# Performance work log

Hardware: AMD Instinct MI355X
Metric: run time of the kernel (lower is better)

The kernel has to match this reference:

```python
import jax, jax.numpy as jnp
import numpy as np

N, E = 50000, 400000
IC, OC, WIDTH, DEPTH = 128, 128, 2, 3


def setup_inputs() -> dict:
    key = jax.random.key(0)
    ks = jax.random.split(key, 9)
    s = 0.02
    return {
        "node_tensor": jax.random.normal(ks[0], (N, 1, IC), jnp.float32),
        "edge_index": jax.random.randint(ks[1], (2, E), 0, N, dtype=jnp.int32),
        "W_pre": jax.random.normal(ks[2], (IC, OC * WIDTH), jnp.float32) * s,
        "b_pre": jax.random.normal(ks[3], (OC * WIDTH,), jnp.float32) * s,
        "W_merge": jax.random.normal(ks[4], (IC, OC * WIDTH), jnp.float32) * s,
        "b_merge": jax.random.normal(ks[5], (OC * WIDTH,), jnp.float32) * s,
        "W_conv": jax.random.normal(ks[6], (WIDTH, OC, OC), jnp.float32) * s,
        "b_conv": jax.random.normal(ks[7], (OC * WIDTH,), jnp.float32) * s,
    }


def reference(node_tensor, edge_index, W_pre, b_pre, W_merge, b_merge, W_conv, b_conv):
    n = node_tensor.shape[0]
    nodes = node_tensor[:, 0, :]                       # (N, IC)

    src, dst = edge_index[0], edge_index[1]
    deg = jax.ops.segment_sum(jnp.ones((E,), node_tensor.dtype), dst, num_segments=n)
    norm = jnp.where(deg > 0, jax.lax.rsqrt(jnp.maximum(deg, 1.0)), 0.0)  # D^{-1/2}

    def laplacian_action(x):                           # x: (N, C); L_sym x
        agg = jax.ops.segment_sum(norm[src, None] * x[src], dst, num_segments=n)
        return x - norm[:, None] * agg

    merge = nodes @ W_merge + b_merge                  # (N, OC*W)
    out = jax.nn.relu(nodes @ W_pre + b_pre + merge)   # (N, OC*W)

    for _ in range(DEPTH - 1):
        out = out - laplacian_action(out)
        # grouped 1x1 conv: width contiguous groups of OC channels
        h = out.reshape(n, WIDTH, OC)
        h = jnp.einsum("nwi,woi->nwo", h, W_conv).reshape(n, WIDTH * OC) + b_conv
        out = jax.nn.relu(h + merge)

    # final (N, OC, W) reshape + adaptive_avg_pool1d(1) == mean over width
    out = out.reshape(n, OC, WIDTH).mean(axis=-1)
    return out[:, :, None]                             # (N, OC, 1)
```

## Files before the change

kernel.cpp:

```cpp
#include <hip/hip_runtime.h>

typedef unsigned short u16;
typedef unsigned char u8;
typedef __attribute__((ext_vector_type(8))) short bf16x8;
typedef __attribute__((ext_vector_type(4))) float f32x4;
typedef __attribute__((ext_vector_type(2))) float f32x2;

#define ICNST 128
#define C2 256

__device__ __forceinline__ float bf2f(u16 u){
  return __uint_as_float(((unsigned int)u) << 16);
}
__device__ __forceinline__ u16 f2bf(float f){
  unsigned int u = __float_as_uint(f);
  unsigned int r = (u + 0x7fffu + ((u >> 16) & 1u)) >> 16;
  return (u16)r;
}
__device__ __forceinline__ unsigned int pk2(float a, float b){
  return (unsigned int)f2bf(a) | ((unsigned int)f2bf(b) << 16);
}

#if defined(__has_builtin)
#if __has_builtin(__builtin_amdgcn_cvt_pk_f32_fp8) && __has_builtin(__builtin_amdgcn_cvt_pk_fp8_f32)
#define HAVE_FP8_BUILTINS 1
#endif
#endif

#ifndef HAVE_FP8_BUILTINS
__device__ __forceinline__ float fp8tof(unsigned int b){
  unsigned int sgn = (b & 0x80u) << 24;
  unsigned int em = b & 0x7fu;
  float mag;
  if (em >= 8u){
    unsigned int e = em >> 3, m = em & 7u;
    mag = __uint_as_float(((e + 120u) << 23) | (m << 20));
  } else {
    mag = (float)em * 0.001953125f;
  }
  return __uint_as_float(__float_as_uint(mag) | sgn);
}
__device__ __forceinline__ unsigned int ftofp8(float f){
  unsigned int u = __float_as_uint(f);
  unsigned int s = (u >> 24) & 0x80u;
  float a = __uint_as_float(u & 0x7fffffffu);
  if (a > 448.f) a = 448.f;
  if (a < 0.015625f){
    int q = (int)(a * 512.f + 0.5f);
    return s | (unsigned int)q;
  }
  int e; float m = frexpf(a, &e);
  int q = (int)(m * 16.f + 0.5f);
  if (q == 16){ q = 8; e += 1; }
  int E = e - 1 + 7;
  if (E > 15){ E = 15; q = 14; }
  return s | (unsigned int)((E << 3) | (q & 7));
}
#endif

template<bool HI>
__device__ __forceinline__ f32x2 up2(unsigned int v){
#ifdef HAVE_FP8_BUILTINS
  return __builtin_amdgcn_cvt_pk_f32_fp8(v, HI);
#else
  f32x2 r;
  constexpr unsigned int sh = HI ? 16u : 0u;
  r.x = fp8tof((v >> sh) & 0xffu);
  r.y = fp8tof((v >> (sh + 8u)) & 0xffu);
  return r;
#endif
}
__device__ __forceinline__ unsigned int pk4fp8(float a, float b, float c, float d){
#ifdef HAVE_FP8_BUILTINS
  unsigned int o = (unsigned int)__builtin_amdgcn_cvt_pk_fp8_f32(a, b, 0, false);
  o = (unsigned int)__builtin_amdgcn_cvt_pk_fp8_f32(c, d, (int)o, true);
  return o;
#else
  return ftofp8(a) | (ftofp8(b) << 8) | (ftofp8(c) << 16) | (ftofp8(d) << 24);
#endif
}

__global__ __launch_bounds__(512) void k_zero(int* __restrict__ deg, int n){
  int i = blockIdx.x * 512 + threadIdx.x;
  if (i < n) deg[i] = 0;
}

__global__ __launch_bounds__(256) void k_pre(const int* __restrict__ dst,
    int* __restrict__ deg, const float* __restrict__ Wpre,
    const float* __restrict__ Wmrg, const float* __restrict__ Wcv,
    u16* __restrict__ WT, u16* __restrict__ Wc, int E){
  int bid = blockIdx.x;
  if (bid < 384){
    int idx = bid * 256 + threadIdx.x;
    if (idx < 65536){
      int j = idx & 511, k = idx >> 9;
      float v = (j < 256) ? Wpre[k * 256 + j] : Wmrg[k * 256 + (j - 256)];
      WT[j * 128 + k] = f2bf(v);
    } else if (idx < 65536 + 32768){
      int x = idx - 65536;
      Wc[x] = f2bf(Wcv[x]);
    }
  } else {
    int e = (bid - 384) * 256 + threadIdx.x;
    if (e < E) atomicAdd(&deg[dst[e]], 1);
  }
}

__global__ __launch_bounds__(256) void k_scan1(const int* __restrict__ deg,
    int* __restrict__ bsum, int n){
  __shared__ int red[256];
  int t = threadIdx.x;
  int i = blockIdx.x * 256 + t;
  red[t] = (i < n) ? deg[i] : 0;
  __syncthreads();
  for (int off = 128; off > 0; off >>= 1){
    if (t < off) red[t] += red[t + off];
    __syncthreads();
  }
  if (t == 0) bsum[blockIdx.x] = red[0];
}

__global__ __launch_bounds__(256) void k_scan2(int* __restrict__ bsum, int nb){
  __shared__ int s[256];
  int t = threadIdx.x;
  int v = (t < nb) ? bsum[t] : 0;
  s[t] = v;
  __syncthreads();
  for (int off = 1; off < 256; off <<= 1){
    int u = (t >= off) ? s[t - off] : 0;
    __syncthreads();
    s[t] += u;
    __syncthreads();
  }
  if (t < nb) bsum[t] = s[t] - v;
}

__global__ __launch_bounds__(256) void k_scan3(const int* __restrict__ deg,
    const int* __restrict__ bsum, int* __restrict__ row_start,
    int* __restrict__ cursor, float* __restrict__ norm, int n){
  __shared__ int s[256];
  int t = threadIdx.x;
  int i = blockIdx.x * 256 + t;
  int v = (i < n) ? deg[i] : 0;
  s[t] = v;
  __syncthreads();
  for (int off = 1; off < 256; off <<= 1){
    int u = (t >= off) ? s[t - off] : 0;
    __syncthreads();
    s[t] += u;
    __syncthreads();
  }
  int ex = s[t] - v + bsum[blockIdx.x];
  if (i < n){
    row_start[i] = ex;
    cursor[i] = ex;
    norm[i] = (v > 0) ? rsqrtf((float)v) : 0.f;
    if (i == n - 1) row_start[n] = ex + v;
  }
}

__global__ void k_scatter(const int* __restrict__ src, const int* __restrict__ dstA,
    int* __restrict__ cursor, int* __restrict__ csr_src, int E){
  int e = blockIdx.x * blockDim.x + threadIdx.x;
  if (e < E){
    int d = dstA[e];
    int pos = atomicAdd(&cursor[d], 1);
    csr_src[pos] = src[e];
  }
}

__global__ __launch_bounds__(512) void k_initM(const float* __restrict__ node,
    const u16* __restrict__ WT, const float* __restrict__ bpre,
    const float* __restrict__ bmrg, const float* __restrict__ norm,
    u16* __restrict__ merge, u8* __restrict__ outA, int n){
  __shared__ u16 Al[64 * 128];
  int t = threadIdx.x;
  int w = t >> 6, l = t & 63;
  int n0 = blockIdx.x * 64;
  int cb = w * 32;
  int lk = (l >> 4) * 8;

  float nr4[4];
  #pragma unroll
  for (int fr = 0; fr < 4; ++fr){
    int row = n0 + fr * 16 + (l & 15);
    nr4[fr] = (row < n) ? norm[row] : 0.f;
  }
  float4 bPr[2], bMr[2];
  #pragma unroll
  for (int fcp = 0; fcp < 2; ++fcp){
    int j0 = cb + fcp * 16 + (l >> 4) * 4;
    bPr[fcp] = *(const float4*)(bpre + j0);
    bMr[fcp] = *(const float4*)(bmrg + j0);
  }

  {
    int row = t >> 3, c0 = (t & 7) * 16;
    const float* src = node + (size_t)(n0 + row) * ICNST + c0;
    bool ok = (n0 + row) < n;
    #pragma unroll
    for (int q = 0; q < 4; ++q){
      float4 v = ok ? *(const float4*)(src + q * 4) : float4{0.f, 0.f, 0.f, 0.f};
      int byte = (row * 256 + c0 * 2 + q * 8) ^ ((row & 7) << 4);
      uint2 pp; pp.x = pk2(v.x, v.y); pp.y = pk2(v.z, v.w);
      *(uint2*)((char*)Al + byte) = pp;
    }
  }
  __syncthreads();

  f32x4 acc[4][4] = {};
  #pragma unroll
  for (int ks = 0; ks < 4; ++ks){
    bf16x8 bf[4];
    #pragma unroll
    for (int fc = 0; fc < 4; ++fc){
      int j = (fc < 2) ? (cb + fc * 16 + (l & 15))
                       : (256 + cb + (fc - 2) * 16 + (l & 15));
      bf[fc] = *(const bf16x8*)(WT + (size_t)j * 128 + ks * 32 + lk);
    }
    bf16x8 af[4];
    #pragma unroll
    for (int fr = 0; fr < 4; ++fr){
      int row = fr * 16 + (l & 15);
      int byte = (row * 256 + ks * 64 + (l >> 4) * 16) ^ ((l & 7) << 4);
      af[fr] = *(const bf16x8*)((const char*)Al + byte);
    }
    #pragma unroll
    for (int fr = 0; fr < 4; ++fr)
      #pragma unroll
      for (int fc = 0; fc < 4; ++fc)
        acc[fr][fc] = __builtin_amdgcn_mfma_f32_16x16x32_bf16(bf[fc], af[fr], acc[fr][fc], 0, 0, 0);
  }

  #pragma unroll
  for (int fr = 0; fr < 4; ++fr){
    int row = n0 + fr * 16 + (l & 15);
    bool ok = row < n;
    float nr = nr4[fr];
    #pragma unroll
    for (int fcp = 0; fcp < 2; ++fcp){
      int j0 = cb + fcp * 16 + (l >> 4) * 4;
      f32x4 aP = acc[fr][fcp], aM = acc[fr][fcp + 2];
      float bPe[4] = {bPr[fcp].x, bPr[fcp].y, bPr[fcp].z, bPr[fcp].w};
      float bMe[4] = {bMr[fcp].x, bMr[fcp].y, bMr[fcp].z, bMr[fcp].w};
      ushort4 mgv;
      u16* mgp = (u16*)&mgv;
      float o4[4];
      #pragma unroll
      for (int r = 0; r < 4; ++r){
        float mg = aM[r] + bMe[r];
        float o  = aP[r] + bPe[r] + mg;
        o = (o > 0.f) ? o : 0.f;
        mgp[r] = f2bf(mg);
        o4[r] = nr * o;
      }
      if (ok){
        *(ushort4*)(merge + (size_t)row * C2 + j0) = mgv;
        *(unsigned int*)(outA + (size_t)row * C2 + j0) = pk4fp8(o4[0], o4[1], o4[2], o4[3]);
      }
    }
  }
}

template<int FINAL>
__global__ __launch_bounds__(512) void k_pconv(const u8* __restrict__ src,
    const int* __restrict__ row_start, const int* __restrict__ csr,
    const float* __restrict__ norm,
    const u16* __restrict__ Wc, const float* __restrict__ bc,
    const u16* __restrict__ merge,
    u8* __restrict__ dstB, float* __restrict__ out, int n, int Etot){
  __shared__ u16 Al[64 * 256];
  int t = threadIdx.x;
  int w = t >> 6, l = t & 63;
  int n0 = blockIdx.x * 64;
  int wh = w >> 2;
  int lk = (l >> 4) * 8;
  int q = l >> 4;
  int c16 = l & 15;

  float nr4[4];
  #pragma unroll
  for (int fr = 0; fr < 4; ++fr){
    int row = n0 + fr * 16 + (l & 15);
    nr4[fr] = (row < n) ? norm[row] : 0.f;
  }
  float4 bCr[2];
  #pragma unroll
  for (int fc = 0; fc < 2; ++fc)
    bCr[fc] = *(const float4*)(bc + w * 32 + fc * 16 + (l >> 4) * 4);

  const u8* Ac = src + (size_t)c16 * 16;
  int rbase = w * 8 + q * 2;
  float acc16[2][16];
  int bb[2], ee[2];
  float ndk[2];
  #pragma unroll
  for (int k = 0; k < 2; ++k){
    int gw = n0 + rbase + k;
    bool ok = gw < n;
    bb[k] = ok ? row_start[gw] : 0;
    ee[k] = ok ? row_start[gw + 1] : 0;
    ndk[k] = ok ? norm[gw] : 0.f;
    #pragma unroll
    for (int m = 0; m < 16; ++m) acc16[k][m] = 0.f;
  }
  int Em1 = Etot - 1;
  bool more = (bb[0] < ee[0]) | (bb[1] < ee[1]);
  while (__any(more)){
    uint4 rr[2];
    float wk[2];
    #pragma unroll
    for (int k = 0; k < 2; ++k){
      bool v = bb[k] < ee[k];
      wk[k] = v ? 1.f : 0.f;
      int idx = (bb[k] < Em1) ? bb[k] : Em1;
      int s0 = csr[idx];
      rr[k] = *(const uint4*)(Ac + (size_t)s0 * C2);
      bb[k] += v ? 1 : 0;
    }
    #pragma unroll
    for (int k = 0; k < 2; ++k){
      f32x2 p;
      p = up2<false>(rr[k].x); acc16[k][ 0] = fmaf(wk[k], p.x, acc16[k][ 0]); acc16[k][ 1] = fmaf(wk[k], p.y, acc16[k][ 1]);
      p = up2<true >(rr[k].x); acc16[k][ 2] = fmaf(wk[k], p.x, acc16[k][ 2]); acc16[k][ 3] = fmaf(wk[k], p.y, acc16[k][ 3]);
      p = up2<false>(rr[k].y); acc16[k][ 4] = fmaf(wk[k], p.x, acc16[k][ 4]); acc16[k][ 5] = fmaf(wk[k], p.y, acc16[k][ 5]);
      p = up2<true >(rr[k].y); acc16[k][ 6] = fmaf(wk[k], p.x, acc16[k][ 6]); acc16[k][ 7] = fmaf(wk[k], p.y, acc16[k][ 7]);
      p = up2<false>(rr[k].z); acc16[k][ 8] = fmaf(wk[k], p.x, acc16[k][ 8]); acc16[k][ 9] = fmaf(wk[k], p.y, acc16[k][ 9]);
      p = up2<true >(rr[k].z); acc16[k][10] = fmaf(wk[k], p.x, acc16[k][10]); acc16[k][11] = fmaf(wk[k], p.y, acc16[k][11]);
      p = up2<false>(rr[k].w); acc16[k][12] = fmaf(wk[k], p.x, acc16[k][12]); acc16[k][13] = fmaf(wk[k], p.y, acc16[k][13]);
      p = up2<true >(rr[k].w); acc16[k][14] = fmaf(wk[k], p.x, acc16[k][14]); acc16[k][15] = fmaf(wk[k], p.y, acc16[k][15]);
    }
    more = (bb[0] < ee[0]) | (bb[1] < ee[1]);
  }
  #pragma unroll
  for (int k = 0; k < 2; ++k){
    int rl = rbase + k;
    float nd = ndk[k];
    uint4 v0, v1;
    v0.x = pk2(nd * acc16[k][ 0], nd * acc16[k][ 1]);
    v0.y = pk2(nd * acc16[k][ 2], nd * acc16[k][ 3]);
    v0.z = pk2(nd * acc16[k][ 4], nd * acc16[k][ 5]);
    v0.w = pk2(nd * acc16[k][ 6], nd * acc16[k][ 7]);
    v1.x = pk2(nd * acc16[k][ 8], nd * acc16[k][ 9]);
    v1.y = pk2(nd * acc16[k][10], nd * acc16[k][11]);
    v1.z = pk2(nd * acc16[k][12], nd * acc16[k][13]);
    v1.w = pk2(nd * acc16[k][14], nd * acc16[k][15]);
    int base2 = rl * 512 + c16 * 32;
    int sw = (rl & 7) << 4;
    *(uint4*)((char*)Al + (base2 ^ sw)) = v0;
    *(uint4*)((char*)Al + ((base2 + 16) ^ sw)) = v1;
  }
  __syncthreads();

  f32x4 acc[4][2] = {};
  #pragma unroll
  for (int ks = 0; ks < 4; ++ks){
    bf16x8 bf[2];
    #pragma unroll
    for (int fc = 0; fc < 2; ++fc){
      int rw = w * 32 + fc * 16 + (l & 15);
      bf[fc] = *(const bf16x8*)(Wc + (size_t)rw * 128 + ks * 32 + lk);
    }
    bf16x8 af[4];
    #pragma unroll
    for (int fr = 0; fr < 4; ++fr){
      int row = fr * 16 + (l & 15);
      int byte = (row * 512 + wh * 256 + ks * 64 + (l >> 4) * 16) ^ ((l & 7) << 4);
      af[fr] = *(const bf16x8*)((const char*)Al + byte);
    }
    #pragma unroll
    for (int fr = 0; fr < 4; ++fr)
      #pragma unroll
      for (int fc = 0; fc < 2; ++fc)
        acc[fr][fc] = __builtin_amdgcn_mfma_f32_16x16x32_bf16(bf[fc], af[fr], acc[fr][fc], 0, 0, 0);
  }

  #pragma unroll
  for (int fr = 0; fr < 4; ++fr){
    int row = n0 + fr * 16 + (l & 15);
    bool ok = row < n;
    float nr = nr4[fr];
    #pragma unroll
    for (int fc = 0; fc < 2; ++fc){
      int j0 = w * 32 + fc * 16 + (l >> 4) * 4;
      ushort4 mg4 = ok ? *(const ushort4*)(merge + (size_t)row * C2 + j0)
                       : ushort4{0, 0, 0, 0};
      const u16* mge = (const u16*)&mg4;
      float bCe[4] = {bCr[fc].x, bCr[fc].y, bCr[fc].z, bCr[fc].w};
      float v[4];
      #pragma unroll
      for (int r = 0; r < 4; ++r){
        float o = acc[fr][fc][r] + bCe[r] + bf2f(mge[r]);
        v[r] = (o > 0.f) ? o : 0.f;
      }
      if (ok){
        if (!FINAL){
          *(unsigned int*)(dstB + (size_t)row * C2 + j0) =
              pk4fp8(nr * v[0], nr * v[1], nr * v[2], nr * v[3]);
        } else {
          float2 om;
          om.x = 0.5f * (v[0] + v[1]);
          om.y = 0.5f * (v[2] + v[3]);
          *(float2*)(out + (size_t)row * 128 + (j0 >> 1)) = om;
        }
      }
    }
  }
}

extern "C" void kernel_launch(void* const* d_in, const int* in_sizes, int n_in,
                              void* d_out, int out_size, void* d_ws, size_t ws_size,
                              hipStream_t stream){
  const float* node = (const float*)d_in[0];
  const int*   eidx = (const int*)d_in[1];
  const float* Wpre = (const float*)d_in[2];
  const float* bpre = (const float*)d_in[3];
  const float* Wmrg = (const float*)d_in[4];
  const float* bmrg = (const float*)d_in[5];
  const float* Wcv  = (const float*)d_in[6];
  const float* bcv  = (const float*)d_in[7];
  float* out = (float*)d_out;

  const int n = in_sizes[0] / ICNST;
  const int E = in_sizes[1] / 2;
  const int* srcp = eidx;
  const int* dstp = eidx + E;

  char* ws = (char*)d_ws;
  size_t off = 0;
  auto alloc = [&](size_t bytes) -> char* {
    char* p = ws + off;
    off += bytes;
    off = (off + 255) & ~(size_t)255;
    return p;
  };
  int*   deg       = (int*)  alloc((size_t)n * 4);
  float* norm      = (float*)alloc((size_t)n * 4);
  int*   row_start = (int*)  alloc((size_t)(n + 1) * 4);
  int*   cursor    = (int*)  alloc((size_t)n * 4);
  int*   csr       = (int*)  alloc((size_t)E * 4);
  u16*   merge     = (u16*)  alloc((size_t)n * C2 * 2);
  u8*    bufA      = (u8*)   alloc((size_t)n * C2);
  u8*    bufB      = (u8*)   alloc((size_t)n * C2);
  u16*   WT        = (u16*)  alloc((size_t)512 * 128 * 2);
  u16*   Wcbf      = (u16*)  alloc((size_t)2 * 128 * 128 * 2);
  int*   bsum      = (int*)  alloc((size_t)256 * 4);
  (void)ws_size; (void)n_in; (void)out_size;

  const int nb = (n + 255) / 256;

  k_zero<<<(n + 511) / 512, 512, 0, stream>>>(deg, n);
  k_pre<<<384 + (E + 255) / 256, 256, 0, stream>>>(dstp, deg, Wpre, Wmrg, Wcv, WT, Wcbf, E);
  k_scan1<<<nb, 256, 0, stream>>>(deg, bsum, n);
  k_scan2<<<1, 256, 0, stream>>>(bsum, nb);
  k_scan3<<<nb, 256, 0, stream>>>(deg, bsum, row_start, cursor, norm, n);
  k_scatter<<<(E + 255) / 256, 256, 0, stream>>>(srcp, dstp, cursor, csr, E);

  int gb64 = (n + 63) / 64;
  k_initM<<<gb64, 512, 0, stream>>>(node, WT, bpre, bmrg, norm, merge, bufA, n);

  k_pconv<0><<<gb64, 512, 0, stream>>>(bufA, row_start, csr, norm, Wcbf, bcv, merge, bufB, nullptr, n, E);
  k_pconv<1><<<gb64, 512, 0, stream>>>(bufB, row_start, csr, norm, Wcbf, bcv, merge, nullptr, out, n, E);
}
```

Baseline: 192.3 us.

## Fuse graph preprocessing kernels into one cooperative kernel with grid syncs

Replaces the zero, weight-conversion/degree, three scan and scatter kernels with a single cooperative kernel on a fixed 256x256 grid. Phases are separated by grid-wide barriers. The aim is to remove several kernel launches and their inter-kernel gaps. In exchange it adds five grid syncs and relies on cooperative launch, with a fixed grid that limits parallelism for the edge passes.

```diff
diff --git a/kernel.cpp b/kernel.cpp
--- a/kernel.cpp
+++ b/kernel.cpp
@@ -1,4 +1,7 @@
 #include <hip/hip_runtime.h>
+#include <hip/hip_cooperative_groups.h>
+
+namespace cg = cooperative_groups;
 
 typedef unsigned short u16;
 typedef unsigned char u8;
@@ -80,50 +83,37 @@
 #endif
 }
 
-__global__ __launch_bounds__(512) void k_zero(int* __restrict__ deg, int n){
-  int i = blockIdx.x * 512 + threadIdx.x;
-  if (i < n) deg[i] = 0;
-}
-
-__global__ __launch_bounds__(256) void k_pre(const int* __restrict__ dst,
+__global__ void k_prep(const int* __restrict__ srcp, const int* __restrict__ dstp,
     int* __restrict__ deg, const float* __restrict__ Wpre,
     const float* __restrict__ Wmrg, const float* __restrict__ Wcv,
-    u16* __restrict__ WT, u16* __restrict__ Wc, int E){
-  int bid = blockIdx.x;
-  if (bid < 384){
-    int idx = bid * 256 + threadIdx.x;
-    if (idx < 65536){
-      int j = idx & 511, k = idx >> 9;
-      float v = (j < 256) ? Wpre[k * 256 + j] : Wmrg[k * 256 + (j - 256)];
-      WT[j * 128 + k] = f2bf(v);
-    } else if (idx < 65536 + 32768){
-      int x = idx - 65536;
-      Wc[x] = f2bf(Wcv[x]);
-    }
-  } else {
-    int e = (bid - 384) * 256 + threadIdx.x;
-    if (e < E) atomicAdd(&deg[dst[e]], 1);
-  }
-}
-
-__global__ __launch_bounds__(256) void k_scan1(const int* __restrict__ deg,
-    int* __restrict__ bsum, int n){
-  __shared__ int red[256];
-  int t = threadIdx.x;
-  int i = blockIdx.x * 256 + t;
-  red[t] = (i < n) ? deg[i] : 0;
-  __syncthreads();
-  for (int off = 128; off > 0; off >>= 1){
-    if (t < off) red[t] += red[t + off];
-    __syncthreads();
-  }
-  if (t == 0) bsum[blockIdx.x] = red[0];
-}
-
-__global__ __launch_bounds__(256) void k_scan2(int* __restrict__ bsum, int nb){
+    u16* __restrict__ WT, u16* __restrict__ Wc,
+    int* __restrict__ row_start, int* __restrict__ cursor,
+    float* __restrict__ norm, int* __restrict__ bsum,
+    int* __restrict__ csr, int n, int E){
+  cg::grid_group grid = cg::this_grid();
   __shared__ int s[256];
-  int t = threadIdx.x;
-  int v = (t < nb) ? bsum[t] : 0;
+  __shared__ int s2[256];
+  int t = threadIdx.x, b = blockIdx.x;
+  int gid = b * 256 + t;
+  const int gsz = 256 * 256;
+
+  for (int i = gid; i < n; i += gsz) deg[i] = 0;
+  grid.sync();
+
+  {
+    int i = gid;
+    int j = i & 511, k = i >> 9;
+    float v = (j < 256) ? Wpre[k * 256 + j] : Wmrg[k * 256 + (j - 256)];
+    WT[j * 128 + k] = f2bf(v);
+  }
+  if (gid < 32768) Wc[gid] = f2bf(Wcv[gid]);
+  for (int e = gid; e < E; e += gsz) atomicAdd(&deg[dstp[e]], 1);
+  grid.sync();
+
+  int C = (n + 255) >> 8;
+  int base = b * C;
+  int v = 0;
+  if (t < C && base + t < n) v = deg[base + t];
   s[t] = v;
   __syncthreads();
   for (int off = 1; off < 256; off <<= 1){
@@ -132,40 +122,39 @@
     s[t] += u;
     __syncthreads();
   }
-  if (t < nb) bsum[t] = s[t] - v;
-}
-
-__global__ __launch_bounds__(256) void k_scan3(const int* __restrict__ deg,
-    const int* __restrict__ bsum, int* __restrict__ row_start,
-    int* __restrict__ cursor, float* __restrict__ norm, int n){
-  __shared__ int s[256];
-  int t = threadIdx.x;
-  int i = blockIdx.x * 256 + t;
-  int v = (i < n) ? deg[i] : 0;
-  s[t] = v;
-  __syncthreads();
-  for (int off = 1; off < 256; off <<= 1){
-    int u = (t >= off) ? s[t - off] : 0;
+  if (t == 255) bsum[b] = s[255];
+  grid.sync();
+
+  if (b == 0){
+    int v2 = bsum[t];
+    s2[t] = v2;
     __syncthreads();
-    s[t] += u;
-    __syncthreads();
-  }
-  int ex = s[t] - v + bsum[blockIdx.x];
-  if (i < n){
-    row_start[i] = ex;
-    cursor[i] = ex;
-    norm[i] = (v > 0) ? rsqrtf((float)v) : 0.f;
-    if (i == n - 1) row_start[n] = ex + v;
-  }
-}
-
-__global__ void k_scatter(const int* __restrict__ src, const int* __restrict__ dstA,
-    int* __restrict__ cursor, int* __restrict__ csr_src, int E){
-  int e = blockIdx.x * blockDim.x + threadIdx.x;
-  if (e < E){
-    int d = dstA[e];
+    for (int off = 1; off < 256; off <<= 1){
+      int u = (t >= off) ? s2[t - off] : 0;
+      __syncthreads();
+      s2[t] += u;
+      __syncthreads();
+    }
+    bsum[t] = s2[t] - v2;
+  }
+  grid.sync();
+
+  {
+    int i = base + t;
+    int ex = s[t] - v + bsum[b];
+    if (t < C && i < n){
+      row_start[i] = ex;
+      cursor[i] = ex;
+      norm[i] = (v > 0) ? rsqrtf((float)v) : 0.f;
+      if (i == n - 1) row_start[n] = ex + v;
+    }
+  }
+  grid.sync();
+
+  for (int e = gid; e < E; e += gsz){
+    int d = dstp[e];
     int pos = atomicAdd(&cursor[d], 1);
-    csr_src[pos] = src[e];
+    csr[pos] = srcp[e];
   }
 }
 
@@ -447,14 +436,14 @@
   int*   bsum      = (int*)  alloc((size_t)256 * 4);
   (void)ws_size; (void)n_in; (void)out_size;
 
-  const int nb = (n + 255) / 256;
-
-  k_zero<<<(n + 511) / 512, 512, 0, stream>>>(deg, n);
-  k_pre<<<384 + (E + 255) / 256, 256, 0, stream>>>(dstp, deg, Wpre, Wmrg, Wcv, WT, Wcbf, E);
-  k_scan1<<<nb, 256, 0, stream>>>(deg, bsum, n);
-  k_scan2<<<1, 256, 0, stream>>>(bsum, nb);
-  k_scan3<<<nb, 256, 0, stream>>>(deg, bsum, row_start, cursor, norm, n);
-  k_scatter<<<(E + 255) / 256, 256, 0, stream>>>(srcp, dstp, cursor, csr, E);
+  {
+    void* args[] = {
+      (void*)&srcp, (void*)&dstp, (void*)&deg, (void*)&Wpre, (void*)&Wmrg,
+      (void*)&Wcv, (void*)&WT, (void*)&Wcbf, (void*)&row_start, (void*)&cursor,
+      (void*)&norm, (void*)&bsum, (void*)&csr, (void*)&n, (void*)&E
+    };
+    hipLaunchCooperativeKernel((void*)k_prep, dim3(256), dim3(256), args, 0, stream);
+  }
 
   int gb64 = (n + 63) / 64;
   k_initM<<<gb64, 512, 0, stream>>>(node, WT, bpre, bmrg, norm, merge, bufA, n);
```

After: 326.7 us. +69.8%, slower.
